# Performance work log

Hardware: AMD Instinct MI355X
Metric: run time of the kernel (lower is better)

The kernel has to match this reference:

```python
import jax, jax.numpy as jnp
import numpy as np

N, C = 32768, 1000

def setup_inputs() -> dict:
    key = jax.random.key(0)
    k1, k2, k3 = jax.random.split(key, 3)
    out = jax.random.normal(k1, (N, C), dtype=jnp.float32)
    T = jax.random.uniform(k2, (C, C), dtype=jnp.float32)
    target = jax.random.randint(k3, (N,), 0, C, dtype=jnp.int64)
    return {"out": out, "T": T, "target": target}

def reference(out, T, target):
    # out: [N, C] logits, T: [C, C] transition matrix, target: [N] int labels
    n = out.shape[0]
    rows = jnp.arange(n)
    log_sm = jax.nn.log_softmax(out, axis=1)          # [N, C]
    sm = jnp.exp(log_sm)                              # softmax(out)
    pro1 = sm[rows, target]                           # softmax[i, y_i]
    # out_T[i] = T^T @ sm[i]  ->  out_T = sm @ T ; pro2 = out_T[i, y_i]
    pro2 = (sm @ T)[rows, target]
    # beta is detached in the original (Variable(...) breaks the graph)
    beta = jax.lax.stop_gradient(pro1 / pro2)         # [N]
    ce = -log_sm[rows, target]                        # per-sample cross entropy
    loss = jnp.sum(beta * ce) / n
    return loss
```

## Files before the change

### kernel.cpp

```cpp
#include <hip/hip_runtime.h>
#include <hip/hip_bf16.h>
#include <float.h>

#define RL_N 32768
#define RL_C 1000
#define NVEC 250
#define TILE 32

#define ROW_BLOCKS 2048
#define WPB 4
#define TOTAL_WAVES (ROW_BLOCKS * WPB)
#define RPW (RL_N / TOTAL_WAVES)

typedef float v4f __attribute__((ext_vector_type(4)));

__device__ __forceinline__ v4f ntload4(const float* p) {
  return __builtin_nontemporal_load((const v4f*)p);
}
__device__ __forceinline__ v4f ld4(const float* p) {
  return *(const v4f*)p;
}

__global__ __launch_bounds__(256) void transpose_kernel(
    const float* __restrict__ in, float* __restrict__ outp, int n) {
  __shared__ float tile[TILE][TILE + 1];
  int x = blockIdx.x * TILE + threadIdx.x;
  int y = blockIdx.y * TILE + threadIdx.y;
#pragma unroll
  for (int k = 0; k < TILE; k += 8) {
    int yy = y + k;
    if (x < n && yy < n) tile[threadIdx.y + k][threadIdx.x] = in[(size_t)yy * n + x];
  }
  __syncthreads();
  x = blockIdx.y * TILE + threadIdx.x;
  y = blockIdx.x * TILE + threadIdx.y;
#pragma unroll
  for (int k = 0; k < TILE; k += 8) {
    int yy = y + k;
    if (x < n && yy < n) outp[(size_t)yy * n + x] = tile[threadIdx.x][threadIdx.y + k];
  }
}

__device__ __forceinline__ float wredsum_l0(float v) {
#pragma unroll
  for (int o = 32; o > 0; o >>= 1) v += __shfl_down(v, o, 64);
  return v;
}

__global__ __launch_bounds__(256) void row_kernel(
    const float* __restrict__ logits, const float* __restrict__ Tt,
    const int* __restrict__ target, float* __restrict__ partial) {
  const int tid  = threadIdx.x;
  const int lane = tid & 63;
  const int wid  = tid >> 6;
  const int wave = blockIdx.x * WPB + wid;
  const int row0 = wave * RPW;

  const bool tail = lane < (NVEC - 192);

  int ys[RPW];
#pragma unroll
  for (int r = 0; r < RPW; ++r) ys[r] = target[row0 + r];

  const v4f NEGBIG = {-FLT_MAX, -FLT_MAX, -FLT_MAX, -FLT_MAX};
  const v4f ZERO4  = {0.f, 0.f, 0.f, 0.f};

  v4f ov[2][4], tv[2][4];

  {
    const float* o = logits + (size_t)row0 * RL_C;
    const float* t = Tt + (size_t)ys[0] * RL_C;
    ov[0][0] = ntload4(o + 4 * lane);
    ov[0][1] = ntload4(o + 4 * (lane + 64));
    ov[0][2] = ntload4(o + 4 * (lane + 128));
    ov[0][3] = tail ? ntload4(o + 4 * (lane + 192)) : NEGBIG;
    tv[0][0] = ld4(t + 4 * lane);
    tv[0][1] = ld4(t + 4 * (lane + 64));
    tv[0][2] = ld4(t + 4 * (lane + 128));
    tv[0][3] = tail ? ld4(t + 4 * (lane + 192)) : ZERO4;
  }

  float s1[RPW], s2[RPW], oy[RPW];

#pragma unroll
  for (int r = 0; r < RPW; ++r) {
    const int cur = r & 1, nxt = cur ^ 1;

    if (r + 1 < RPW) {
      const float* o = logits + (size_t)(row0 + r + 1) * RL_C;
      const float* t = Tt + (size_t)ys[r + 1] * RL_C;
      ov[nxt][0] = ntload4(o + 4 * lane);
      ov[nxt][1] = ntload4(o + 4 * (lane + 64));
      ov[nxt][2] = ntload4(o + 4 * (lane + 128));
      ov[nxt][3] = tail ? ntload4(o + 4 * (lane + 192)) : NEGBIG;
      tv[nxt][0] = ld4(t + 4 * lane);
      tv[nxt][1] = ld4(t + 4 * (lane + 64));
      tv[nxt][2] = ld4(t + 4 * (lane + 128));
      tv[nxt][3] = tail ? ld4(t + 4 * (lane + 192)) : ZERO4;
    }

    float a1 = 0.f, a2 = 0.f;
#pragma unroll
    for (int k = 0; k < 4; ++k) {
      float ex = __expf(ov[cur][k].x);
      float ey = __expf(ov[cur][k].y);
      float ez = __expf(ov[cur][k].z);
      float ew = __expf(ov[cur][k].w);
      a1 += (ex + ey) + (ez + ew);
      a2 += (ex * tv[cur][k].x + ey * tv[cur][k].y)
          + (ez * tv[cur][k].z + ew * tv[cur][k].w);
    }
    s1[r] = a1;
    s2[r] = a2;

    const int v = ys[r] >> 2;
    const int c = v >> 6;
    const int owner = v & 63;
    const int comp = ys[r] & 3;
    v4f f = (c == 0) ? ov[cur][0] : (c == 1) ? ov[cur][1]
          : (c == 2) ? ov[cur][2] : ov[cur][3];
    float sel = (comp == 0) ? f.x : (comp == 1) ? f.y : (comp == 2) ? f.z : f.w;
    oy[r] = __shfl(sel, owner, 64);
  }

  float s1t[RPW], s2t[RPW];
#pragma unroll
  for (int r = 0; r < RPW; ++r) {
    s1t[r] = wredsum_l0(s1[r]);
    s2t[r] = wredsum_l0(s2[r]);
  }

  float acc = 0.f;
  if (lane == 0) {
#pragma unroll
    for (int r = 0; r < RPW; ++r) {
      const float beta = __expf(oy[r]) / s2t[r];
      const float ce   = __logf(s1t[r]) - oy[r];
      acc += beta * ce;
    }
  }

  __shared__ float sm[WPB];
  if (lane == 0) sm[wid] = acc;
  __syncthreads();
  if (tid == 0) partial[blockIdx.x] = (sm[0] + sm[1]) + (sm[2] + sm[3]);
}

__global__ __launch_bounds__(256) void reduce_kernel(
    const float* __restrict__ partial, float* __restrict__ outp, float inv_n) {
  const int tid  = threadIdx.x;
  const int lane = tid & 63;
  const int wid  = tid >> 6;
  float s = 0.f;
#pragma unroll
  for (int i = tid; i < ROW_BLOCKS; i += 256) s += partial[i];
  float ws = wredsum_l0(s);
  __shared__ float sm[4];
  if (lane == 0) sm[wid] = ws;
  __syncthreads();
  if (tid == 0) outp[0] = ((sm[0] + sm[1]) + (sm[2] + sm[3])) * inv_n;
}

extern "C" void kernel_launch(void* const* d_in, const int* in_sizes, int n_in,
                              void* d_out, int out_size, void* d_ws, size_t ws_size,
                              hipStream_t stream) {
  const float* logits = (const float*)d_in[0];
  const float* T      = (const float*)d_in[1];
  const int*   target = (const int*)d_in[2];
  float* outp = (float*)d_out;

  float* Tt      = (float*)d_ws;
  float* partial = (float*)((char*)d_ws + (size_t)RL_C * RL_C * sizeof(float));

  dim3 tb(TILE, 8);
  dim3 tg((RL_C + TILE - 1) / TILE, (RL_C + TILE - 1) / TILE);
  transpose_kernel<<<tg, tb, 0, stream>>>(T, Tt, RL_C);

  row_kernel<<<ROW_BLOCKS, 256, 0, stream>>>(logits, Tt, target, partial);

  reduce_kernel<<<1, 256, 0, stream>>>(partial, outp, 1.0f / (float)RL_N);
}
```

Before: 193.7 us.

## Sort rows by target class so waves reuse the same T row

Adds a counting sort of rows by target label (histogram, prefix scan and scatter kernels), and row_kernel processes rows in that permuted order. Rows sharing a label then land in the same wave or neighbouring waves, so the gathered transposed-T row is more likely to hit in cache. The cost is three extra small kernel launches plus an indirect, non-sequential read of logits rows. Because atomics decide the order inside each label bucket, the summation order can vary between runs.

```diff
diff --git a/kernel.cpp b/kernel.cpp
--- a/kernel.cpp
+++ b/kernel.cpp
@@ -17,12 +17,14 @@
 __device__ __forceinline__ v4f ntload4(const float* p) {
   return __builtin_nontemporal_load((const v4f*)p);
 }
-__device__ __forceinline__ v4f ld4(const float* p) {
-  return *(const v4f*)p;
-}
+__device__ __forceinline__ v4f ld4(const float* p) { return *(const v4f*)p; }
 
 __global__ __launch_bounds__(256) void transpose_kernel(
-    const float* __restrict__ in, float* __restrict__ outp, int n) {
+    const float* __restrict__ in, float* __restrict__ outp,
+    int* __restrict__ bins, int n) {
+  if (blockIdx.x == 0 && blockIdx.y == 0) {
+    for (int i = threadIdx.y * TILE + threadIdx.x; i < RL_C; i += 256) bins[i] = 0;
+  }
   __shared__ float tile[TILE][TILE + 1];
   int x = blockIdx.x * TILE + threadIdx.x;
   int y = blockIdx.y * TILE + threadIdx.y;
@@ -41,6 +43,46 @@
   }
 }
 
+#define HIST_BLOCKS 64
+#define HIST_THREADS 512
+__global__ __launch_bounds__(HIST_THREADS) void hist_kernel(
+    const int* __restrict__ target, int* __restrict__ bins) {
+  __shared__ int h[RL_C];
+  for (int i = threadIdx.x; i < RL_C; i += HIST_THREADS) h[i] = 0;
+  __syncthreads();
+  const int i = blockIdx.x * HIST_THREADS + threadIdx.x;
+  atomicAdd(&h[target[i]], 1);
+  __syncthreads();
+  for (int i2 = threadIdx.x; i2 < RL_C; i2 += HIST_THREADS)
+    if (h[i2]) atomicAdd(&bins[i2], h[i2]);
+}
+
+__global__ __launch_bounds__(1024) void scan_kernel(
+    const int* __restrict__ bins, int* __restrict__ offsets) {
+  __shared__ int s[1024];
+  const int tid = threadIdx.x;
+  const int own = (tid < RL_C) ? bins[tid] : 0;
+  s[tid] = own;
+#pragma unroll
+  for (int off = 1; off < 1024; off <<= 1) {
+    __syncthreads();
+    int v = (tid >= off) ? s[tid - off] : 0;
+    __syncthreads();
+    s[tid] += v;
+  }
+  __syncthreads();
+  if (tid < RL_C) offsets[tid] = s[tid] - own;
+}
+
+__global__ __launch_bounds__(256) void scatter_kernel(
+    const int* __restrict__ target, int* __restrict__ offsets,
+    int* __restrict__ perm) {
+  const int i = blockIdx.x * 256 + threadIdx.x;
+  const int y = target[i];
+  const int pos = atomicAdd(&offsets[y], 1);
+  perm[pos] = i;
+}
+
 __device__ __forceinline__ float wredsum_l0(float v) {
 #pragma unroll
   for (int o = 32; o > 0; o >>= 1) v += __shfl_down(v, o, 64);
@@ -49,7 +91,8 @@
 
 __global__ __launch_bounds__(256) void row_kernel(
     const float* __restrict__ logits, const float* __restrict__ Tt,
-    const int* __restrict__ target, float* __restrict__ partial) {
+    const int* __restrict__ target, const int* __restrict__ perm,
+    float* __restrict__ partial) {
   const int tid  = threadIdx.x;
   const int lane = tid & 63;
   const int wid  = tid >> 6;
@@ -58,9 +101,12 @@
 
   const bool tail = lane < (NVEC - 192);
 
-  int ys[RPW];
-#pragma unroll
-  for (int r = 0; r < RPW; ++r) ys[r] = target[row0 + r];
+  int rows[RPW], ys[RPW];
+#pragma unroll
+  for (int r = 0; r < RPW; ++r) {
+    rows[r] = perm[row0 + r];
+    ys[r]   = target[rows[r]];
+  }
 
   const v4f NEGBIG = {-FLT_MAX, -FLT_MAX, -FLT_MAX, -FLT_MAX};
   const v4f ZERO4  = {0.f, 0.f, 0.f, 0.f};
@@ -68,7 +114,7 @@
   v4f ov[2][4], tv[2][4];
 
   {
-    const float* o = logits + (size_t)row0 * RL_C;
+    const float* o = logits + (size_t)rows[0] * RL_C;
     const float* t = Tt + (size_t)ys[0] * RL_C;
     ov[0][0] = ntload4(o + 4 * lane);
     ov[0][1] = ntload4(o + 4 * (lane + 64));
@@ -87,7 +133,7 @@
     const int cur = r & 1, nxt = cur ^ 1;
 
     if (r + 1 < RPW) {
-      const float* o = logits + (size_t)(row0 + r + 1) * RL_C;
+      const float* o = logits + (size_t)rows[r + 1] * RL_C;
       const float* t = Tt + (size_t)ys[r + 1] * RL_C;
       ov[nxt][0] = ntload4(o + 4 * lane);
       ov[nxt][1] = ntload4(o + 4 * (lane + 64));
@@ -169,14 +215,22 @@
   const int*   target = (const int*)d_in[2];
   float* outp = (float*)d_out;
 
-  float* Tt      = (float*)d_ws;
-  float* partial = (float*)((char*)d_ws + (size_t)RL_C * RL_C * sizeof(float));
+  char* ws = (char*)d_ws;
+  float* Tt      = (float*)(ws);
+  float* partial = (float*)(ws + 4000000);
+  int*   bins    = (int*)(ws + 4008192);
+  int*   offsets = (int*)(ws + 4012192);
+  int*   perm    = (int*)(ws + 4016192);
 
   dim3 tb(TILE, 8);
   dim3 tg((RL_C + TILE - 1) / TILE, (RL_C + TILE - 1) / TILE);
-  transpose_kernel<<<tg, tb, 0, stream>>>(T, Tt, RL_C);
-
-  row_kernel<<<ROW_BLOCKS, 256, 0, stream>>>(logits, Tt, target, partial);
+  transpose_kernel<<<tg, tb, 0, stream>>>(T, Tt, bins, RL_C);
+
+  hist_kernel<<<HIST_BLOCKS, HIST_THREADS, 0, stream>>>(target, bins);
+  scan_kernel<<<1, 1024, 0, stream>>>(bins, offsets);
+  scatter_kernel<<<RL_N / 256, 256, 0, stream>>>(target, offsets, perm);
+
+  row_kernel<<<ROW_BLOCKS, 256, 0, stream>>>(logits, Tt, target, perm, partial);
 
   reduce_kernel<<<1, 256, 0, stream>>>(partial, outp, 1.0f / (float)RL_N);
 }
```

Measured after the change: 208.6 us. +7.7%, slower.
